# Kernel optimization log

Hardware: AMD Instinct MI355X
Metric: run time of the kernel (lower is better)

Reference implementation:

```python
import jax, jax.numpy as jnp
import numpy as np

N = 50000        # nodes
E = 1500000      # edges
D = 128          # hidden_dim
L = 3            # layers_mp (t = 0..L-1)
RBAR = 1         # cfg.rbar -> delay = max(k - RBAR, 0)
EPS = 0.0        # GIN epsilon (not trainable)


def setup_inputs() -> dict:
    key = jax.random.key(0)
    ks = jax.random.split(key, 6)
    x = jax.random.normal(ks[0], (N, D), dtype=jnp.float32)
    edge_index = jax.random.randint(ks[1], (2, E), 0, N)          # [2, E] src/dst
    edge_attr = jax.random.randint(ks[2], (E,), 0, L)             # relation id k-1 in {0..L-1}
    # per-layer mlp_s: Linear(D, D) + ReLU
    Ws_s = jax.random.normal(ks[3], (L, D, D), dtype=jnp.float32) / np.float32(np.sqrt(D))
    bs_s = jnp.zeros((L, D), dtype=jnp.float32)
    # per-layer, per-relation mlp_k[k-1]: Linear(D, D) + ReLU (layer t uses k = 1..t+1)
    Ws_k = jax.random.normal(ks[4], (L, L, D, D), dtype=jnp.float32) / np.float32(np.sqrt(D))
    bs_k = jnp.zeros((L, L, D), dtype=jnp.float32)
    return dict(x=x, Ws_s=Ws_s, bs_s=bs_s, Ws_k=Ws_k, bs_k=bs_k,
                edge_index=edge_index, edge_attr=edge_attr)


def reference(x, Ws_s, bs_s, Ws_k, bs_k, edge_index, edge_attr):
    src, dst = edge_index[0], edge_index[1]
    n = x.shape[0]
    xs = []
    for t in range(L):
        xs.append(x)
        out = None
        for k in range(1, t + 2):
            delay = max(k - RBAR, 0)
            h_src = xs[t - delay]                       # delayed history for relation k
            # edge-type-grouped scatter-add: mask edges of relation k, gather, segment-sum
            mask = (edge_attr == (k - 1))
            msg = jnp.where(mask[:, None], h_src[src], jnp.float32(0.0))   # [E, D]
            agg = jax.ops.segment_sum(msg, dst, num_segments=n)            # [N, D]
            h = jax.nn.relu(agg @ Ws_k[t, k - 1] + bs_k[t, k - 1])         # mlp_k[k-1]
            out = h if out is None else out + h
        # self term: (1 + eps) * mlp_s(x); nn_post is identity (empty Sequential)
        out = out + (1.0 + EPS) * jax.nn.relu(x @ Ws_s[t] + bs_s[t])
        # outer loop: ReLU, dropout(p=0, eval), residual
        x = xs[-1] + jax.nn.relu(out)
    return x
```

## Files before the change

### kernel.cpp

```cpp
#include <hip/hip_runtime.h>

#define NN 50000
#define NE 1500000
#define DD 128
#define NRANGE ((NN + 255) / 256)
#define NBUCK (3 * NRANGE)
#define BINB 256
#define CHUNK ((NE + BINB - 1) / BINB)
#define NH2 (NBUCK * BINB)

typedef __attribute__((ext_vector_type(8))) short short8;
typedef __attribute__((ext_vector_type(4))) float f32x4;

__device__ __forceinline__ ushort f2b(float x) {
    uint u = __float_as_uint(x);
    u += 0x7FFFu + ((u >> 16) & 1u);
    return (ushort)(u >> 16);
}
__device__ __forceinline__ float b2f(ushort b) {
    return __uint_as_float(((uint)b) << 16);
}

__global__ __launch_bounds__(256) void scan_block(
    const int* __restrict__ cnt, int* __restrict__ ptr, int* __restrict__ part, int n)
{
    __shared__ int s[256];
    int i = blockIdx.x * 256 + threadIdx.x;
    int v = (i < n) ? cnt[i] : 0;
    s[threadIdx.x] = v;
    __syncthreads();
    #pragma unroll
    for (int off = 1; off < 256; off <<= 1) {
        int t = (threadIdx.x >= off) ? s[threadIdx.x - off] : 0;
        __syncthreads();
        s[threadIdx.x] += t;
        __syncthreads();
    }
    if (i < n) ptr[i] = s[threadIdx.x] - v;
    if (threadIdx.x == 255) part[blockIdx.x] = s[255];
}

__global__ void scan_partials(int* __restrict__ part, int nb)
{
    int lane = threadIdx.x;
    int run = 0;
    for (int base = 0; base < nb; base += 64) {
        int i = base + lane;
        int v = (i < nb) ? part[i] : 0;
        int x = v;
        #pragma unroll
        for (int off = 1; off < 64; off <<= 1) {
            int t = __shfl_up(x, off);
            if (lane >= off) x += t;
        }
        if (i < nb) part[i] = run + x - v;
        run += __shfl(x, 63);
    }
}

__global__ __launch_bounds__(256) void scan_add(
    int* __restrict__ ptr, const int* __restrict__ part, int n)
{
    int i = blockIdx.x * 256 + threadIdx.x;
    if (i >= n) return;
    ptr[i] += part[blockIdx.x];
}

__global__ __launch_bounds__(256) void histB(
    const int* __restrict__ dst, const int* __restrict__ attr, int* __restrict__ hist2)
{
    __shared__ int lh[NBUCK];
    int tid = threadIdx.x, blk = blockIdx.x;
    for (int i = tid; i < NBUCK; i += 256) lh[i] = 0;
    __syncthreads();
    int lo = blk * CHUNK, hi = lo + CHUNK; if (hi > NE) hi = NE;
    for (int e = lo + tid; e < hi; e += 256)
        atomicAdd(&lh[attr[e] * NRANGE + (dst[e] >> 8)], 1);
    __syncthreads();
    for (int i = tid; i < NBUCK; i += 256) hist2[i * BINB + blk] = lh[i];
}

__global__ __launch_bounds__(256) void binB(
    const int* __restrict__ src, const int* __restrict__ dst, const int* __restrict__ attr,
    const int* __restrict__ off2, uint* __restrict__ binned)
{
    __shared__ int lc[NBUCK];
    int tid = threadIdx.x, blk = blockIdx.x;
    for (int i = tid; i < NBUCK; i += 256) lc[i] = off2[i * BINB + blk];
    __syncthreads();
    int lo = blk * CHUNK, hi = lo + CHUNK; if (hi > NE) hi = NE;
    for (int e = lo + tid; e < hi; e += 256) {
        int d = dst[e];
        int b = attr[e] * NRANGE + (d >> 8);
        int pos = atomicAdd(&lc[b], 1);
        binned[pos] = (uint)src[e] | ((uint)(d & 255) << 16);
    }
}

__global__ __launch_bounds__(256) void bucket_finalize(
    const uint* __restrict__ binned, const int* __restrict__ off2,
    int* __restrict__ ptr, int* __restrict__ ssrc)
{
    __shared__ int lh[256];
    __shared__ int sc[256];
    __shared__ int cur[256];
    int b = blockIdx.x, tid = threadIdx.x;
    int rel = b / NRANGE, r0 = (b % NRANGE) << 8;
    int nloc = NN - r0; if (nloc > 256) nloc = 256;
    int lo = off2[b * BINB];
    int hi = (b + 1 < NBUCK) ? off2[(b + 1) * BINB] : NE;
    lh[tid] = 0;
    __syncthreads();
    for (int e = lo + tid; e < hi; e += 256)
        atomicAdd(&lh[(binned[e] >> 16) & 255], 1);
    __syncthreads();
    int v = lh[tid];
    sc[tid] = v;
    __syncthreads();
    #pragma unroll
    for (int off = 1; off < 256; off <<= 1) {
        int t = (tid >= off) ? sc[tid - off] : 0;
        __syncthreads();
        sc[tid] += t;
        __syncthreads();
    }
    int excl = lo + sc[tid] - v;
    if (tid < nloc) ptr[rel * NN + r0 + tid] = excl;
    cur[tid] = excl;
    if (b == NBUCK - 1 && tid == 0) ptr[3 * NN] = NE;
    __syncthreads();
    for (int e = lo + tid; e < hi; e += 256) {
        uint p = binned[e];
        int pos = atomicAdd(&cur[(p >> 16) & 255], 1);
        ssrc[pos] = p & 0xFFFFu;
    }
}

__global__ __launch_bounds__(256) void prep_w(
    const float* __restrict__ Ws_s, const float* __restrict__ Ws_k, ushort* __restrict__ wt)
{
    int i = blockIdx.x * 256 + threadIdx.x;
    if (i >= 9 * 4096) return;
    int m = i >> 12;
    int f = (i & 4095) * 4;
    int k = f >> 7, n = f & 127;
    const int tk[6] = {0, 3, 4, 6, 7, 8};
    const float* W = (m < 3) ? (Ws_s + (size_t)m * 16384)
                             : (Ws_k + (size_t)tk[m - 3] * 16384);
    float4 v = *(const float4*)(W + (size_t)k * DD + n);
    ushort* o = wt + (size_t)m * 16384 + k;
    o[(size_t)(n + 0) * DD] = f2b(v.x);
    o[(size_t)(n + 1) * DD] = f2b(v.y);
    o[(size_t)(n + 2) * DD] = f2b(v.z);
    o[(size_t)(n + 3) * DD] = f2b(v.w);
}

__global__ __launch_bounds__(256) void to_bf16(
    const float* __restrict__ x, ushort* __restrict__ xb)
{
    int i = blockIdx.x * 256 + threadIdx.x;
    if (i >= NN * DD / 4) return;
    float4 v = ((const float4*)x)[i];
    ushort4 o;
    o.x = f2b(v.x); o.y = f2b(v.y); o.z = f2b(v.z); o.w = f2b(v.w);
    ((ushort4*)xb)[i] = o;
}

__global__ __launch_bounds__(256) void gather_multi(
    const ushort* __restrict__ h0, const ushort* __restrict__ h1,
    const ushort* __restrict__ h2,
    const int* __restrict__ ptr, const int* __restrict__ ssrc,
    ushort* __restrict__ agg0, ushort* __restrict__ agg1, ushort* __restrict__ agg2)
{
    int rel = blockIdx.y;
    const ushort* h = (rel == 0) ? h0 : ((rel == 1) ? h1 : h2);
    ushort* agg     = (rel == 0) ? agg0 : ((rel == 1) ? agg1 : agg2);

    int n = blockIdx.x * 4 + (threadIdx.x >> 6);
    if (n >= NN) return;
    int lane = threadIdx.x & 63;
    const int* p = ptr + rel * NN + n;
    int s0 = __builtin_amdgcn_readfirstlane(p[0]);
    int s1 = __builtin_amdgcn_readfirstlane(p[1]);
    float a0 = 0.f, a1 = 0.f, c0 = 0.f, c1 = 0.f;
    int e = s0;
    for (; e + 8 <= s1; e += 8) {
        int idx[8];
        #pragma unroll
        for (int j = 0; j < 8; ++j) idx[j] = ssrc[e + j];
        uint v[8];
        #pragma unroll
        for (int j = 0; j < 8; ++j)
            v[j] = ((const uint*)(h + (size_t)idx[j] * DD))[lane];
        #pragma unroll
        for (int j = 0; j < 8; j += 2) {
            a0 += b2f((ushort)(v[j] & 0xFFFFu));     a1 += b2f((ushort)(v[j] >> 16));
            c0 += b2f((ushort)(v[j + 1] & 0xFFFFu)); c1 += b2f((ushort)(v[j + 1] >> 16));
        }
    }
    for (; e + 4 <= s1; e += 4) {
        int i0 = ssrc[e], i1 = ssrc[e + 1], i2 = ssrc[e + 2], i3 = ssrc[e + 3];
        uint v0 = ((const uint*)(h + (size_t)i0 * DD))[lane];
        uint v1 = ((const uint*)(h + (size_t)i1 * DD))[lane];
        uint v2 = ((const uint*)(h + (size_t)i2 * DD))[lane];
        uint v3 = ((const uint*)(h + (size_t)i3 * DD))[lane];
        a0 += b2f((ushort)(v0 & 0xFFFFu)); a1 += b2f((ushort)(v0 >> 16));
        c0 += b2f((ushort)(v1 & 0xFFFFu)); c1 += b2f((ushort)(v1 >> 16));
        a0 += b2f((ushort)(v2 & 0xFFFFu)); a1 += b2f((ushort)(v2 >> 16));
        c0 += b2f((ushort)(v3 & 0xFFFFu)); c1 += b2f((ushort)(v3 >> 16));
    }
    for (; e < s1; ++e) {
        int s = ssrc[e];
        uint v = ((const uint*)(h + (size_t)s * DD))[lane];
        a0 += b2f((ushort)(v & 0xFFFFu)); a1 += b2f((ushort)(v >> 16));
    }
    a0 += c0; a1 += c1;
    uint o = (uint)f2b(a0) | ((uint)f2b(a1) << 16);
    ((uint*)(agg + (size_t)n * DD))[lane] = o;
}

template<int NSRC, int WRITEB>
__global__ __launch_bounds__(256) void layer_mm(
    const ushort* __restrict__ s0, const ushort* __restrict__ s1,
    const ushort* __restrict__ s2, const ushort* __restrict__ s3,
    const ushort* __restrict__ w0, const ushort* __restrict__ w1,
    const ushort* __restrict__ w2, const ushort* __restrict__ w3,
    const float* __restrict__ b0, const float* __restrict__ b1,
    const float* __restrict__ b2, const float* __restrict__ b3,
    const float* __restrict__ xold, float* __restrict__ xnew, ushort* __restrict__ xbnew)
{
    __shared__ ushort Atile[64 * 128];
    const int tid  = threadIdx.x;
    const int wave = tid >> 6, lane = tid & 63;
    const int row0 = blockIdx.x * 64;

    const ushort* srcs[4] = { s0, s1, s2, s3 };
    const ushort* wts[4]  = { w0, w1, w2, w3 };
    const float*  bss[4]  = { b0, b1, b2, b3 };

    float facc[4][2][4];
    #pragma unroll
    for (int rt = 0; rt < 4; ++rt)
        #pragma unroll
        for (int ct = 0; ct < 2; ++ct)
            #pragma unroll
            for (int q = 0; q < 4; ++q) facc[rt][ct][q] = 0.f;

    #pragma unroll
    for (int sidx = 0; sidx < NSRC; ++sidx) {
        const ushort* S = srcs[sidx];
        const ushort* W = wts[sidx];

        __syncthreads();
        for (int i = tid; i < 1024; i += 256) {
            int r = i >> 4, c = i & 15;
            int gr = row0 + r;
            uint4 v = make_uint4(0, 0, 0, 0);
            if (gr < NN) v = ((const uint4*)(S + (size_t)gr * DD))[c];
            int byte = ((r << 8) + (c << 4)) ^ ((r & 7) << 4);
            *((uint4*)((char*)Atile + byte)) = v;
        }
        short8 bfr[2][4];
        #pragma unroll
        for (int ct = 0; ct < 2; ++ct)
            #pragma unroll
            for (int ks = 0; ks < 4; ++ks) {
                int col = (wave << 5) + (ct << 4) + (lane & 15);
                int kb  = (ks << 5) + ((lane >> 4) << 3);
                bfr[ct][ks] = *(const short8*)(W + (size_t)col * DD + kb);
            }
        __syncthreads();

        f32x4 c[4][2];
        #pragma unroll
        for (int rt = 0; rt < 4; ++rt)
            #pragma unroll
            for (int ct = 0; ct < 2; ++ct) c[rt][ct] = (f32x4)(0.f);

        #pragma unroll
        for (int rt = 0; rt < 4; ++rt) {
            int row = (rt << 4) + (lane & 15);
            #pragma unroll
            for (int ks = 0; ks < 4; ++ks) {
                int byte = ((row << 8) + (ks << 6) + ((lane >> 4) << 4)) ^ ((row & 7) << 4);
                short8 a = *((const short8*)((const char*)Atile + byte));
                c[rt][0] = __builtin_amdgcn_mfma_f32_16x16x32_bf16(a, bfr[0][ks], c[rt][0], 0, 0, 0);
                c[rt][1] = __builtin_amdgcn_mfma_f32_16x16x32_bf16(a, bfr[1][ks], c[rt][1], 0, 0, 0);
            }
        }

        const float* B = bss[sidx];
        #pragma unroll
        for (int ct = 0; ct < 2; ++ct) {
            float bb = B[(wave << 5) + (ct << 4) + (lane & 15)];
            #pragma unroll
            for (int rt = 0; rt < 4; ++rt)
                #pragma unroll
                for (int q = 0; q < 4; ++q) {
                    float v = c[rt][ct][q] + bb;
                    facc[rt][ct][q] += v > 0.f ? v : 0.f;
                }
        }
    }

    #pragma unroll
    for (int rt = 0; rt < 4; ++rt)
        #pragma unroll
        for (int q = 0; q < 4; ++q) {
            int row = row0 + (rt << 4) + ((lane >> 4) << 2) + q;
            if (row >= NN) continue;
            #pragma unroll
            for (int ct = 0; ct < 2; ++ct) {
                int col = (wave << 5) + (ct << 4) + (lane & 15);
                size_t off = (size_t)row * DD + col;
                float v = facc[rt][ct][q] + xold[off];
                xnew[off] = v;
                if (WRITEB) xbnew[off] = f2b(v);
            }
        }
}

extern "C" void kernel_launch(void* const* d_in, const int* in_sizes, int n_in,
                              void* d_out, int out_size, void* d_ws, size_t ws_size,
                              hipStream_t stream) {
    const float* x0   = (const float*)d_in[0];
    const float* Ws_s = (const float*)d_in[1];
    const float* bs_s = (const float*)d_in[2];
    const float* Ws_k = (const float*)d_in[3];
    const float* bs_k = (const float*)d_in[4];
    const int*   src  = (const int*)d_in[5];
    const int*   dst  = src + NE;
    const int*   attr = (const int*)d_in[6];
    float* out = (float*)d_out;

    float*  x1   = (float*)d_ws;
    ushort* xb0  = (ushort*)(x1 + (size_t)NN * DD);
    ushort* xb1  = xb0 + (size_t)NN * DD;
    ushort* xb2  = xb1 + (size_t)NN * DD;
    ushort* agg0 = xb2 + (size_t)NN * DD;
    ushort* agg1 = agg0 + (size_t)NN * DD;
    ushort* agg2 = agg1 + (size_t)NN * DD;
    ushort* wtb  = agg2 + (size_t)NN * DD;
    int* ptr    = (int*)(wtb + 9 * 16384);
    int* hist2  = ptr + 3 * NN + 1;
    int* off2   = hist2 + NH2;
    int* part2  = off2 + NH2;
    int* ssrc   = part2 + 1024;
    uint* binned = (uint*)agg0;

    const int gGemm = (NN + 63) / 64;
    const int gGath = (NN + 3) / 4;
    const int gConv = (NN * DD / 4 + 255) / 256;
    const int NB2 = (NH2 + 255) / 256;

    auto wt = [&](int m) { return wtb + (size_t)m * 16384; };
    auto bk = [&](int t, int k) { return bs_k + ((size_t)t * 3 + k) * DD; };

    histB<<<BINB, 256, 0, stream>>>(dst, attr, hist2);
    scan_block<<<NB2, 256, 0, stream>>>(hist2, off2, part2, NH2);
    scan_partials<<<1, 64, 0, stream>>>(part2, NB2);
    scan_add<<<NB2, 256, 0, stream>>>(off2, part2, NH2);
    binB<<<BINB, 256, 0, stream>>>(src, dst, attr, off2, binned);
    bucket_finalize<<<NBUCK, 256, 0, stream>>>(binned, off2, ptr, ssrc);
    prep_w<<<144, 256, 0, stream>>>(Ws_s, Ws_k, wtb);
    to_bf16<<<gConv, 256, 0, stream>>>(x0, xb0);

    gather_multi<<<dim3(gGath, 1), 256, 0, stream>>>(
        xb0, nullptr, nullptr, ptr, ssrc, agg0, nullptr, nullptr);
    layer_mm<2, 1><<<gGemm, 256, 0, stream>>>(
        xb0, agg0, nullptr, nullptr,
        wt(0), wt(3), nullptr, nullptr,
        bs_s, bk(0, 0), nullptr, nullptr,
        x0, x1, xb1);

    gather_multi<<<dim3(gGath, 2), 256, 0, stream>>>(
        xb1, xb0, nullptr, ptr, ssrc, agg0, agg1, nullptr);
    layer_mm<3, 1><<<gGemm, 256, 0, stream>>>(
        xb1, agg0, agg1, nullptr,
        wt(1), wt(4), wt(5), nullptr,
        bs_s + DD, bk(1, 0), bk(1, 1), nullptr,
        x1, out, xb2);

    gather_multi<<<dim3(gGath, 3), 256, 0, stream>>>(
        xb2, xb1, xb0, ptr, ssrc, agg0, agg1, agg2);
    layer_mm<4, 0><<<gGemm, 256, 0, stream>>>(
        xb2, agg0, agg1, agg2,
        wt(2), wt(6), wt(7), wt(8),
        bs_s + 2 * DD, bk(2, 0), bk(2, 1), bk(2, 2),
        out, out, nullptr);
}
```

Before: 278.4 us.

## Gather each history once across layers and store edge sources as 16-bit

Since agg for relation k depends only on the delayed history, each aggregation result is computed when its source history first appears. Gathers are then issued from a single source tensor, so each launch reads one feature table, which should improve cache locality. The results are kept in persistent workspace buffers for later layers, and the scratch used to build the CSR is aliased onto those buffers. The sorted source index array also shrinks to ushort, halving its reads, which relies on node ids fitting in 16 bits (N=50000).

```diff
diff --git a/kernel.cpp b/kernel.cpp
--- a/kernel.cpp
+++ b/kernel.cpp
@@ -99,7 +99,7 @@
 
 __global__ __launch_bounds__(256) void bucket_finalize(
     const uint* __restrict__ binned, const int* __restrict__ off2,
-    int* __restrict__ ptr, int* __restrict__ ssrc)
+    int* __restrict__ ptr, ushort* __restrict__ ssrc)
 {
     __shared__ int lh[256];
     __shared__ int sc[256];
@@ -132,7 +132,7 @@
     for (int e = lo + tid; e < hi; e += 256) {
         uint p = binned[e];
         int pos = atomicAdd(&cur[(p >> 16) & 255], 1);
-        ssrc[pos] = p & 0xFFFFu;
+        ssrc[pos] = (ushort)(p & 0xFFFFu);
     }
 }
 
@@ -167,14 +167,12 @@
 }
 
 __global__ __launch_bounds__(256) void gather_multi(
-    const ushort* __restrict__ h0, const ushort* __restrict__ h1,
-    const ushort* __restrict__ h2,
-    const int* __restrict__ ptr, const int* __restrict__ ssrc,
-    ushort* __restrict__ agg0, ushort* __restrict__ agg1, ushort* __restrict__ agg2)
+    const ushort* __restrict__ h,
+    const int* __restrict__ ptr, const ushort* __restrict__ ssrc,
+    ushort* __restrict__ a0, ushort* __restrict__ a1, ushort* __restrict__ a2)
 {
     int rel = blockIdx.y;
-    const ushort* h = (rel == 0) ? h0 : ((rel == 1) ? h1 : h2);
-    ushort* agg     = (rel == 0) ? agg0 : ((rel == 1) ? agg1 : agg2);
+    ushort* agg = (rel == 0) ? a0 : ((rel == 1) ? a1 : a2);
 
     int n = blockIdx.x * 4 + (threadIdx.x >> 6);
     if (n >= NN) return;
@@ -182,7 +180,7 @@
     const int* p = ptr + rel * NN + n;
     int s0 = __builtin_amdgcn_readfirstlane(p[0]);
     int s1 = __builtin_amdgcn_readfirstlane(p[1]);
-    float a0 = 0.f, a1 = 0.f, c0 = 0.f, c1 = 0.f;
+    float a0f = 0.f, a1f = 0.f, c0f = 0.f, c1f = 0.f;
     int e = s0;
     for (; e + 8 <= s1; e += 8) {
         int idx[8];
@@ -194,8 +192,8 @@
             v[j] = ((const uint*)(h + (size_t)idx[j] * DD))[lane];
         #pragma unroll
         for (int j = 0; j < 8; j += 2) {
-            a0 += b2f((ushort)(v[j] & 0xFFFFu));     a1 += b2f((ushort)(v[j] >> 16));
-            c0 += b2f((ushort)(v[j + 1] & 0xFFFFu)); c1 += b2f((ushort)(v[j + 1] >> 16));
+            a0f += b2f((ushort)(v[j] & 0xFFFFu));     a1f += b2f((ushort)(v[j] >> 16));
+            c0f += b2f((ushort)(v[j + 1] & 0xFFFFu)); c1f += b2f((ushort)(v[j + 1] >> 16));
         }
     }
     for (; e + 4 <= s1; e += 4) {
@@ -204,18 +202,18 @@
         uint v1 = ((const uint*)(h + (size_t)i1 * DD))[lane];
         uint v2 = ((const uint*)(h + (size_t)i2 * DD))[lane];
         uint v3 = ((const uint*)(h + (size_t)i3 * DD))[lane];
-        a0 += b2f((ushort)(v0 & 0xFFFFu)); a1 += b2f((ushort)(v0 >> 16));
-        c0 += b2f((ushort)(v1 & 0xFFFFu)); c1 += b2f((ushort)(v1 >> 16));
-        a0 += b2f((ushort)(v2 & 0xFFFFu)); a1 += b2f((ushort)(v2 >> 16));
-        c0 += b2f((ushort)(v3 & 0xFFFFu)); c1 += b2f((ushort)(v3 >> 16));
+        a0f += b2f((ushort)(v0 & 0xFFFFu)); a1f += b2f((ushort)(v0 >> 16));
+        c0f += b2f((ushort)(v1 & 0xFFFFu)); c1f += b2f((ushort)(v1 >> 16));
+        a0f += b2f((ushort)(v2 & 0xFFFFu)); a1f += b2f((ushort)(v2 >> 16));
+        c0f += b2f((ushort)(v3 & 0xFFFFu)); c1f += b2f((ushort)(v3 >> 16));
     }
     for (; e < s1; ++e) {
         int s = ssrc[e];
         uint v = ((const uint*)(h + (size_t)s * DD))[lane];
-        a0 += b2f((ushort)(v & 0xFFFFu)); a1 += b2f((ushort)(v >> 16));
-    }
-    a0 += c0; a1 += c1;
-    uint o = (uint)f2b(a0) | ((uint)f2b(a1) << 16);
+        a0f += b2f((ushort)(v & 0xFFFFu)); a1f += b2f((ushort)(v >> 16));
+    }
+    a0f += c0f; a1f += c1f;
+    uint o = (uint)f2b(a0f) | ((uint)f2b(a1f) << 16);
     ((uint*)(agg + (size_t)n * DD))[lane] = o;
 }
 
@@ -337,16 +335,17 @@
     ushort* xb0  = (ushort*)(x1 + (size_t)NN * DD);
     ushort* xb1  = xb0 + (size_t)NN * DD;
     ushort* xb2  = xb1 + (size_t)NN * DD;
-    ushort* agg0 = xb2 + (size_t)NN * DD;
-    ushort* agg1 = agg0 + (size_t)NN * DD;
-    ushort* agg2 = agg1 + (size_t)NN * DD;
-    ushort* wtb  = agg2 + (size_t)NN * DD;
+    ushort* P0   = xb2 + (size_t)NN * DD;
+    ushort* P1   = P0 + (size_t)NN * DD;
+    ushort* P2   = P1 + (size_t)NN * DD;
+    ushort* P3   = P2 + (size_t)NN * DD;
+    ushort* wtb  = P3 + (size_t)NN * DD;
     int* ptr    = (int*)(wtb + 9 * 16384);
-    int* hist2  = ptr + 3 * NN + 1;
-    int* off2   = hist2 + NH2;
-    int* part2  = off2 + NH2;
-    int* ssrc   = part2 + 1024;
-    uint* binned = (uint*)agg0;
+    int* part2  = ptr + 3 * NN + 1;
+    ushort* ssrc = (ushort*)(part2 + 1024);
+    int* hist2  = (int*)P1;
+    int* off2   = (int*)P2;
+    uint* binned = (uint*)P3;
 
     const int gGemm = (NN + 63) / 64;
     const int gGath = (NN + 3) / 4;
@@ -365,26 +364,23 @@
     prep_w<<<144, 256, 0, stream>>>(Ws_s, Ws_k, wtb);
     to_bf16<<<gConv, 256, 0, stream>>>(x0, xb0);
 
-    gather_multi<<<dim3(gGath, 1), 256, 0, stream>>>(
-        xb0, nullptr, nullptr, ptr, ssrc, agg0, nullptr, nullptr);
+    gather_multi<<<dim3(gGath, 3), 256, 0, stream>>>(xb0, ptr, ssrc, P0, P1, P3);
     layer_mm<2, 1><<<gGemm, 256, 0, stream>>>(
-        xb0, agg0, nullptr, nullptr,
+        xb0, P0, nullptr, nullptr,
         wt(0), wt(3), nullptr, nullptr,
         bs_s, bk(0, 0), nullptr, nullptr,
         x0, x1, xb1);
 
-    gather_multi<<<dim3(gGath, 2), 256, 0, stream>>>(
-        xb1, xb0, nullptr, ptr, ssrc, agg0, agg1, nullptr);
+    gather_multi<<<dim3(gGath, 2), 256, 0, stream>>>(xb1, ptr, ssrc, P0, P2, nullptr);
     layer_mm<3, 1><<<gGemm, 256, 0, stream>>>(
-        xb1, agg0, agg1, nullptr,
+        xb1, P0, P1, nullptr,
         wt(1), wt(4), wt(5), nullptr,
         bs_s + DD, bk(1, 0), bk(1, 1), nullptr,
         x1, out, xb2);
 
-    gather_multi<<<dim3(gGath, 3), 256, 0, stream>>>(
-        xb2, xb1, xb0, ptr, ssrc, agg0, agg1, agg2);
+    gather_multi<<<dim3(gGath, 1), 256, 0, stream>>>(xb2, ptr, ssrc, P0, nullptr, nullptr);
     layer_mm<4, 0><<<gGemm, 256, 0, stream>>>(
-        xb2, agg0, agg1, agg2,
+        xb2, P0, P2, P3,
         wt(2), wt(6), wt(7), wt(8),
         bs_s + 2 * DD, bk(2, 0), bk(2, 1), bk(2, 2),
         out, out, nullptr);
```

Result: slower. 298.5 us (+7.2%).
